# Optimization experiments

Measured on AMD Instinct MI355X. Metric: run time of the kernel, lower is better.

Reference implementation:

```python
import jax, jax.numpy as jnp
import numpy as np

B, L, D = 2, 2048, 1024
H, FD, HD = 16, 16, 64  # num_heads, feature_dim, head_dim
EPS = 1e-12


def setup_inputs() -> dict:
    key = jax.random.key(0)
    ks = jax.random.split(key, 5)
    s = 0.02
    return {
        "hidden_states": jax.random.normal(ks[0], (B, L, D), jnp.float32),
        "Wq": jax.random.normal(ks[1], (H * FD, D), jnp.float32) * s,
        "Wk": jax.random.normal(ks[2], (H * FD, D), jnp.float32) * s,
        "Wv": jax.random.normal(ks[3], (H * HD, D), jnp.float32) * s,
        "Wo": jax.random.normal(ks[4], (D, H * HD), jnp.float32) * s,
    }


def reference(hidden_states, Wq, Wk, Wv, Wo):
    b, l, _ = hidden_states.shape
    # projections (nn.Linear: y = x @ W.T), split heads -> (b, h, l, d)
    q = (hidden_states @ Wq.T).reshape(b, l, H, FD).transpose(0, 2, 1, 3)
    k = (hidden_states @ Wk.T).reshape(b, l, H, FD).transpose(0, 2, 1, 3)
    v = (hidden_states @ Wv.T).reshape(b, l, H, HD).transpose(0, 2, 1, 3)
    # feature_map is identity
    # quadratic causal linear attention
    A = jnp.einsum('bhnd,bhmd->bhnm', q, k)  # (b,h,l,l)
    causal = jnp.tril(jnp.ones((l, l), dtype=bool))
    A = jnp.where(causal, A, jnp.zeros((), A.dtype))
    y = jnp.einsum('bhnm,bhme->bhne', A, v)  # (b,h,l,hd)
    # causal cumsum normalization
    z = 1.0 / (jnp.einsum('bhld,bhld->bhl', q, jnp.cumsum(k, axis=2)) + EPS)
    y = y * z[..., None]
    y = y.transpose(0, 2, 1, 3).reshape(b, l, H * HD)  # b l (h d)
    return y @ Wo.T
```

## Files before the change

### kernel.cpp

```cpp
#include <hip/hip_runtime.h>


#define L_    2048
#define NROW  4096
#define CHUNK 128
#define NCH   16
#define NBH   32
#define K3    3072

typedef __attribute__((ext_vector_type(8))) short short8v;
typedef __attribute__((ext_vector_type(4))) float floatx4;

__device__ __forceinline__ ushort bf_rne(float x) {
    unsigned u = __float_as_uint(x);
    return (ushort)((u + 0x7fffu + ((u >> 16) & 1u)) >> 16);
}
__device__ __forceinline__ float bf_to_f(ushort h) {
    return __uint_as_float(((unsigned)h) << 16);
}
__device__ __forceinline__ void gload16(const ushort* g, ushort* l) {
    __builtin_amdgcn_global_load_lds(
        (const __attribute__((address_space(1))) unsigned int*)g,
        (__attribute__((address_space(3))) unsigned int*)l, 16, 0, 0);
}

__global__ __launch_bounds__(256) void split3(const float* __restrict__ in,
                                              ushort* __restrict__ out3, int nrow,
                                              int lo_off, int hi2_off) {
    int idx = blockIdx.x * 256 + threadIdx.x;
    int row = idx >> 7, g = idx & 127;
    if (row >= nrow) return;
    const float* p = in + (size_t)row * 1024 + g * 8;
    float4 x0 = *(const float4*)p, x1 = *(const float4*)(p + 4);
    float xs[8] = {x0.x, x0.y, x0.z, x0.w, x1.x, x1.y, x1.z, x1.w};
    ushort hs[8], ls[8];
#pragma unroll
    for (int j = 0; j < 8; ++j) {
        ushort h = bf_rne(xs[j]);
        hs[j] = h;
        ls[j] = bf_rne(xs[j] - bf_to_f(h));
    }
    ushort* o = out3 + (size_t)row * 3072 + g * 8;
    ushort4 h0 = make_ushort4(hs[0], hs[1], hs[2], hs[3]);
    ushort4 h1 = make_ushort4(hs[4], hs[5], hs[6], hs[7]);
    *(ushort4*)(o)               = h0;
    *(ushort4*)(o + 4)           = h1;
    *(ushort4*)(o + hi2_off)     = h0;
    *(ushort4*)(o + hi2_off + 4) = h1;
    *(ushort4*)(o + lo_off)      = make_ushort4(ls[0], ls[1], ls[2], ls[3]);
    *(ushort4*)(o + lo_off + 4)  = make_ushort4(ls[4], ls[5], ls[6], ls[7]);
}

__global__ __launch_bounds__(256) void gemm_bf16x3(const ushort* __restrict__ A3,
                                                   const ushort* __restrict__ B3,
                                                   float* __restrict__ Cm, int Nn) {
    __shared__ ushort As[2][8192];
    __shared__ ushort Bs[2][8192];
    const int tid = threadIdx.x;
    const int lane = tid & 63;
    const int wy = tid >> 7;
    const int wx = (tid >> 6) & 1;
    const int m0 = blockIdx.y * 128;
    const int n0 = blockIdx.x * 128;

    const int arow = tid >> 3;
    const int aslot = (tid & 7) ^ (arow & 7);
    const ushort* pA[4];
    const ushort* pB[4];
#pragma unroll
    for (int i = 0; i < 4; ++i) {
        pA[i] = A3 + (size_t)(m0 + i * 32 + arow) * K3 + aslot * 8;
        pB[i] = B3 + (size_t)(n0 + i * 32 + arow) * K3 + aslot * 8;
    }

#define STAGE(buf, kk)                                              \
    do {                                                            \
        _Pragma("unroll") for (int i = 0; i < 4; ++i)               \
            gload16(pA[i] + (kk), &As[buf][i * 2048 + tid * 8]);    \
        _Pragma("unroll") for (int i = 0; i < 4; ++i)               \
            gload16(pB[i] + (kk), &Bs[buf][i * 2048 + tid * 8]);    \
    } while (0)

    const int abase = (wy * 64 + (lane & 15)) * 64;
    const int bbase = (wx * 64 + (lane & 15)) * 64;

    floatx4 acc[4][4] = {};
    STAGE(0, 0);
    for (int t = 0; t < 48; ++t) {
        const int cur = t & 1;
        __syncthreads();
        if (t < 47) STAGE(1 - cur, (t + 1) * 64);
#pragma unroll
        for (int ksub = 0; ksub < 2; ++ksub) {
            const int so = ((((lane >> 4) | (ksub << 2)) ^ (lane & 7)) << 3);
            short8v a[4], b[4];
#pragma unroll
            for (int mf = 0; mf < 4; ++mf)
                a[mf] = *(const short8v*)&As[cur][abase + mf * 1024 + so];
#pragma unroll
            for (int nf = 0; nf < 4; ++nf)
                b[nf] = *(const short8v*)&Bs[cur][bbase + nf * 1024 + so];
#pragma unroll
            for (int mf = 0; mf < 4; ++mf)
#pragma unroll
                for (int nf = 0; nf < 4; ++nf)
                    acc[mf][nf] = __builtin_amdgcn_mfma_f32_16x16x32_bf16(
                        a[mf], b[nf], acc[mf][nf], 0, 0, 0);
        }
    }
#undef STAGE

#pragma unroll
    for (int mf = 0; mf < 4; ++mf) {
        int row = m0 + wy * 64 + mf * 16 + ((lane >> 4) << 2);
#pragma unroll
        for (int nf = 0; nf < 4; ++nf) {
            int col = n0 + wx * 64 + nf * 16 + (lane & 15);
#pragma unroll
            for (int r = 0; r < 4; ++r)
                Cm[(size_t)(row + r) * Nn + col] = acc[mf][nf][r];
        }
    }
}

#define TM 64
#define TN 64
#define TK 32
#define LDP 68

__global__ __launch_bounds__(256) void gemm_qk_f64(const float* __restrict__ X,
                                                   const float* __restrict__ Wq,
                                                   const float* __restrict__ Wk,
                                                   double* __restrict__ q64,
                                                   double* __restrict__ k64) {
    __shared__ float As[TK][LDP];
    __shared__ float Bs[TK][LDP];
    const int tid = threadIdx.x;
    const int m0 = blockIdx.y * TM;
    const int n0g = blockIdx.x * TN;
    const bool isq = n0g < 256;
    const float* Wm = isq ? Wq : Wk;
    double* Cm = isq ? q64 : k64;
    const int n0 = isq ? n0g : n0g - 256;

    const int lr = tid >> 2;
    const int lc = (tid & 3) << 2;
    const int ty = tid >> 4;
    const int tx = tid & 15;

    double acc[4][4] = {};
    const float* Ap = X + (size_t)(m0 + lr) * 1024 + lc;
    const float* Bp = Wm + (size_t)(n0 + lr) * 1024 + lc;

    for (int k0 = 0; k0 < 1024; k0 += TK) {
        float4 a0 = *(const float4*)(Ap + k0);
        float4 a1 = *(const float4*)(Ap + k0 + 16);
        float4 b0 = *(const float4*)(Bp + k0);
        float4 b1 = *(const float4*)(Bp + k0 + 16);
        __syncthreads();
        As[lc + 0][lr] = a0.x; As[lc + 1][lr] = a0.y;
        As[lc + 2][lr] = a0.z; As[lc + 3][lr] = a0.w;
        As[lc + 16][lr] = a1.x; As[lc + 17][lr] = a1.y;
        As[lc + 18][lr] = a1.z; As[lc + 19][lr] = a1.w;
        Bs[lc + 0][lr] = b0.x; Bs[lc + 1][lr] = b0.y;
        Bs[lc + 2][lr] = b0.z; Bs[lc + 3][lr] = b0.w;
        Bs[lc + 16][lr] = b1.x; Bs[lc + 17][lr] = b1.y;
        Bs[lc + 18][lr] = b1.z; Bs[lc + 19][lr] = b1.w;
        __syncthreads();
#pragma unroll
        for (int kk = 0; kk < TK; ++kk) {
            float4 av = *(const float4*)&As[kk][ty << 2];
            float4 bv = *(const float4*)&Bs[kk][tx << 2];
            double a[4] = {(double)av.x, (double)av.y, (double)av.z, (double)av.w};
            double b[4] = {(double)bv.x, (double)bv.y, (double)bv.z, (double)bv.w};
#pragma unroll
            for (int i = 0; i < 4; ++i)
#pragma unroll
                for (int j = 0; j < 4; ++j)
                    acc[i][j] += a[i] * b[j];
        }
    }
#pragma unroll
    for (int i = 0; i < 4; ++i) {
        size_t o = (size_t)(m0 + (ty << 2) + i) * 256 + n0 + (tx << 2);
        double2 r0 = {acc[i][0], acc[i][1]};
        double2 r1 = {acc[i][2], acc[i][3]};
        *(double2*)&Cm[o] = r0;
        *(double2*)&Cm[o + 2] = r1;
    }
}

__global__ __launch_bounds__(256) void chunk_kv(const double* __restrict__ kg,
                                                const float* __restrict__ vg,
                                                float* __restrict__ KV,
                                                double* __restrict__ Ksum) {
    __shared__ double ksd[CHUNK][16];
    __shared__ float vs[CHUNK][64];
    const int c = blockIdx.x, bh = blockIdx.y;
    const int b = bh >> 4, h = bh & 15;
    const int n0 = b * L_ + c * CHUNK;
    const int tid = threadIdx.x;

    {
        int r = tid >> 1, o = (tid & 1) * 8;
        const double* kp = &kg[(size_t)(n0 + r) * 256 + h * 16 + o];
#pragma unroll
        for (int j = 0; j < 4; ++j)
            *(double2*)&ksd[r][o + j * 2] = *(const double2*)(kp + j * 2);
    }
    {
        int r = tid >> 1, half = (tid & 1) * 32;
        const float* vp = &vg[(size_t)(n0 + r) * 1024 + h * 64 + half];
#pragma unroll
        for (int j = 0; j < 8; ++j)
            *(float4*)&vs[r][half + j * 4] = *(const float4*)(vp + j * 4);
    }
    __syncthreads();

    const int f = tid >> 4;
    const int e4 = tid & 15;
    float a0 = 0.f, a1 = 0.f, a2 = 0.f, a3 = 0.f;
    double ksacc = 0.0;
    for (int l = 0; l < CHUNK; ++l) {
        double kd = ksd[l][f];
        float kv = (float)kd;
        float4 vv = *(const float4*)&vs[l][e4 << 2];
        a0 += kv * vv.x; a1 += kv * vv.y; a2 += kv * vv.z; a3 += kv * vv.w;
        ksacc += kd;
    }
    size_t o = ((size_t)bh * NCH + c) * 1024 + f * 64 + (e4 << 2);
    float4 r = {a0, a1, a2, a3};
    *(float4*)&KV[o] = r;
    if (e4 == 0) Ksum[((size_t)bh * NCH + c) * 16 + f] = ksacc;
}

__global__ __launch_bounds__(256) void prefix_kv(const float* __restrict__ KV,
                                                 const double* __restrict__ Ksum,
                                                 float* __restrict__ KVpre,
                                                 double* __restrict__ Kpre) {
    const int bh = blockIdx.x;
    const int t = threadIdx.x;
    float r0 = 0.f, r1 = 0.f, r2 = 0.f, r3 = 0.f;
    size_t base = (size_t)bh * NCH * 1024 + t * 4;
    for (int c = 0; c < NCH; ++c) {
        float4 w = {r0, r1, r2, r3};
        *(float4*)&KVpre[base + (size_t)c * 1024] = w;
        float4 cur = *(const float4*)&KV[base + (size_t)c * 1024];
        r0 += cur.x; r1 += cur.y; r2 += cur.z; r3 += cur.w;
    }
    if (t < 16) {
        double s = 0.0;
        size_t kb = (size_t)bh * NCH * 16 + t;
        for (int c = 0; c < NCH; ++c) {
            Kpre[kb + (size_t)c * 16] = s;
            s += Ksum[kb + (size_t)c * 16];
        }
    }
}

__global__ __launch_bounds__(256) void attn_out(const double* __restrict__ qg,
                                                const double* __restrict__ kg,
                                                const float* __restrict__ vg,
                                                const float* __restrict__ kvpre,
                                                const double* __restrict__ kpreg,
                                                ushort* __restrict__ y3) {
    __shared__ double qs[CHUNK][16];
    __shared__ double ks[CHUNK][16];
    __shared__ float vs[CHUNK][64];
    __shared__ float s0[16][64];
    __shared__ double kp[16];
    const int c = blockIdx.x, bh = blockIdx.y;
    const int b = bh >> 4, h = bh & 15;
    const int n0 = b * L_ + c * CHUNK;
    const int tid = threadIdx.x;

    {
        int r = tid >> 1, o = (tid & 1) * 8;
        const double* qp = &qg[(size_t)(n0 + r) * 256 + h * 16 + o];
        const double* kptr = &kg[(size_t)(n0 + r) * 256 + h * 16 + o];
#pragma unroll
        for (int j = 0; j < 4; ++j) {
            *(double2*)&qs[r][o + j * 2] = *(const double2*)(qp + j * 2);
            *(double2*)&ks[r][o + j * 2] = *(const double2*)(kptr + j * 2);
        }
    }
    {
        int r = tid >> 1, half = (tid & 1) * 32;
        const float* vp = &vg[(size_t)(n0 + r) * 1024 + h * 64 + half];
#pragma unroll
        for (int j = 0; j < 8; ++j)
            *(float4*)&vs[r][half + j * 4] = *(const float4*)(vp + j * 4);
    }
    {
        float4 w = *(const float4*)&kvpre[((size_t)bh * NCH + c) * 1024 + tid * 4];
        *(float4*)&s0[0][tid * 4] = w;
        if (tid < 16) kp[tid] = kpreg[((size_t)bh * NCH + c) * 16 + tid];
    }
    __syncthreads();

    const int i = tid >> 1;
    const int half = (tid & 1) * 32;

    double qr[16];
#pragma unroll
    for (int f = 0; f < 16; ++f) qr[f] = qs[i][f];

    double denom = 0.0;
#pragma unroll
    for (int f = 0; f < 16; ++f) denom += qr[f] * kp[f];

    float acc[32] = {};
#pragma unroll
    for (int f = 0; f < 16; ++f) {
        float qf = (float)qr[f];
#pragma unroll
        for (int e = 0; e < 32; e += 4) {
            float4 sv = *(const float4*)&s0[f][half + e];
            acc[e + 0] += qf * sv.x; acc[e + 1] += qf * sv.y;
            acc[e + 2] += qf * sv.z; acc[e + 3] += qf * sv.w;
        }
    }
    for (int j = 0; j <= i; ++j) {
        double s64 = 0.0;
#pragma unroll
        for (int f = 0; f < 16; ++f) s64 += qr[f] * ks[j][f];
        denom += s64;
        float s = (float)s64;
        const float4* vj = (const float4*)&vs[j][half];
#pragma unroll
        for (int e4 = 0; e4 < 8; ++e4) {
            float4 vv = vj[e4];
            acc[e4 * 4 + 0] += s * vv.x; acc[e4 * 4 + 1] += s * vv.y;
            acc[e4 * 4 + 2] += s * vv.z; acc[e4 * 4 + 3] += s * vv.w;
        }
    }

    const float z = (float)(1.0 / (denom + 1e-12));
    ushort* yp = &y3[(size_t)(n0 + i) * K3 + h * 64 + half];
#pragma unroll
    for (int e4 = 0; e4 < 8; ++e4) {
        ushort hs[4], ls[4];
#pragma unroll
        for (int j = 0; j < 4; ++j) {
            float val = acc[e4 * 4 + j] * z;
            ushort hh = bf_rne(val);
            hs[j] = hh;
            ls[j] = bf_rne(val - bf_to_f(hh));
        }
        ushort4 hv = make_ushort4(hs[0], hs[1], hs[2], hs[3]);
        *(ushort4*)(yp + e4 * 4)        = hv;
        *(ushort4*)(yp + 1024 + e4 * 4) = make_ushort4(ls[0], ls[1], ls[2], ls[3]);
        *(ushort4*)(yp + 2048 + e4 * 4) = hv;
    }
}

extern "C" void kernel_launch(void* const* d_in, const int* in_sizes, int n_in,
                              void* d_out, int out_size, void* d_ws, size_t ws_size,
                              hipStream_t stream) {
    const float* X  = (const float*)d_in[0];
    const float* Wq = (const float*)d_in[1];
    const float* Wk = (const float*)d_in[2];
    const float* Wv = (const float*)d_in[3];
    const float* Wo = (const float*)d_in[4];
    float* out = (float*)d_out;

    double* q64   = (double*)d_ws;
    double* k64   = q64 + 1048576;
    float*  v     = (float*)(k64 + 1048576);
    float*  KV    = v + 4194304;
    float*  KVpre = KV + 524288;
    double* Ksum  = (double*)(KVpre + 524288);
    double* Kpre  = Ksum + 8192;
    ushort* X3    = (ushort*)(Kpre + 8192);
    ushort* Wv3   = X3 + (size_t)4096 * K3;
    ushort* Wo3   = Wv3 + (size_t)1024 * K3;

    dim3 blk(256);
    split3<<<2048, blk, 0, stream>>>(X, X3, 4096, 1024, 2048);
    split3<<<512, blk, 0, stream>>>(Wv, Wv3, 1024, 2048, 1024);
    split3<<<512, blk, 0, stream>>>(Wo, Wo3, 1024, 2048, 1024);
    gemm_qk_f64<<<dim3(8, 64), blk, 0, stream>>>(X, Wq, Wk, q64, k64);
    gemm_bf16x3<<<dim3(8, 32), blk, 0, stream>>>(X3, Wv3, v, 1024);
    chunk_kv<<<dim3(NCH, NBH), blk, 0, stream>>>(k64, v, KV, Ksum);
    prefix_kv<<<dim3(NBH), blk, 0, stream>>>(KV, Ksum, KVpre, Kpre);
    attn_out<<<dim3(NCH, NBH), blk, 0, stream>>>(q64, k64, v, KVpre, Kpre, X3);
    gemm_bf16x3<<<dim3(8, 32), blk, 0, stream>>>(X3, Wo3, out, 1024);
}
```

Baseline: 335.0 us.

## Merge fp64 QK projection and bf16x3 V projection into one heterogeneous launch

The separate fp64 Q/K GEMM and the bf16x3 MFMA V GEMM are combined into a single 768-block kernel. Blocks are interleaved in triples, two running the fp64 QK tile and one running the V tile, so the FP64-ALU-bound and MFMA-bound work share the GPU at the same time and one launch disappears. The cost is that every block now reserves 64 KB of shared memory, which limits occupancy for the QK blocks that only need a small part of it. Register pressure is also set by whichever of the two paths is larger.

```diff
diff --git a/kernel.cpp b/kernel.cpp
--- a/kernel.cpp
+++ b/kernel.cpp
@@ -7,6 +7,11 @@
 #define NCH   16
 #define NBH   32
 #define K3    3072
+
+#define TM 64
+#define TN 64
+#define TK 32
+#define LDP 68
 
 typedef __attribute__((ext_vector_type(8))) short short8v;
 typedef __attribute__((ext_vector_type(4))) float floatx4;
@@ -123,70 +128,144 @@
     }
 }
 
-#define TM 64
-#define TN 64
-#define TK 32
-#define LDP 68
-
-__global__ __launch_bounds__(256) void gemm_qk_f64(const float* __restrict__ X,
-                                                   const float* __restrict__ Wq,
-                                                   const float* __restrict__ Wk,
-                                                   double* __restrict__ q64,
-                                                   double* __restrict__ k64) {
-    __shared__ float As[TK][LDP];
-    __shared__ float Bs[TK][LDP];
+__global__ __launch_bounds__(256) void fused_qk_v(const float* __restrict__ X,
+                                                  const float* __restrict__ Wq,
+                                                  const float* __restrict__ Wk,
+                                                  double* __restrict__ q64,
+                                                  double* __restrict__ k64,
+                                                  const ushort* __restrict__ A3,
+                                                  const ushort* __restrict__ B3,
+                                                  float* __restrict__ Vout) {
+    __shared__ __align__(16) char smem[65536];
     const int tid = threadIdx.x;
-    const int m0 = blockIdx.y * TM;
-    const int n0g = blockIdx.x * TN;
-    const bool isq = n0g < 256;
-    const float* Wm = isq ? Wq : Wk;
-    double* Cm = isq ? q64 : k64;
-    const int n0 = isq ? n0g : n0g - 256;
-
-    const int lr = tid >> 2;
-    const int lc = (tid & 3) << 2;
-    const int ty = tid >> 4;
-    const int tx = tid & 15;
-
-    double acc[4][4] = {};
-    const float* Ap = X + (size_t)(m0 + lr) * 1024 + lc;
-    const float* Bp = Wm + (size_t)(n0 + lr) * 1024 + lc;
-
-    for (int k0 = 0; k0 < 1024; k0 += TK) {
-        float4 a0 = *(const float4*)(Ap + k0);
-        float4 a1 = *(const float4*)(Ap + k0 + 16);
-        float4 b0 = *(const float4*)(Bp + k0);
-        float4 b1 = *(const float4*)(Bp + k0 + 16);
-        __syncthreads();
-        As[lc + 0][lr] = a0.x; As[lc + 1][lr] = a0.y;
-        As[lc + 2][lr] = a0.z; As[lc + 3][lr] = a0.w;
-        As[lc + 16][lr] = a1.x; As[lc + 17][lr] = a1.y;
-        As[lc + 18][lr] = a1.z; As[lc + 19][lr] = a1.w;
-        Bs[lc + 0][lr] = b0.x; Bs[lc + 1][lr] = b0.y;
-        Bs[lc + 2][lr] = b0.z; Bs[lc + 3][lr] = b0.w;
-        Bs[lc + 16][lr] = b1.x; Bs[lc + 17][lr] = b1.y;
-        Bs[lc + 18][lr] = b1.z; Bs[lc + 19][lr] = b1.w;
-        __syncthreads();
-#pragma unroll
-        for (int kk = 0; kk < TK; ++kk) {
-            float4 av = *(const float4*)&As[kk][ty << 2];
-            float4 bv = *(const float4*)&Bs[kk][tx << 2];
-            double a[4] = {(double)av.x, (double)av.y, (double)av.z, (double)av.w};
-            double b[4] = {(double)bv.x, (double)bv.y, (double)bv.z, (double)bv.w};
-#pragma unroll
-            for (int i = 0; i < 4; ++i)
-#pragma unroll
-                for (int j = 0; j < 4; ++j)
-                    acc[i][j] += a[i] * b[j];
-        }
-    }
-#pragma unroll
-    for (int i = 0; i < 4; ++i) {
-        size_t o = (size_t)(m0 + (ty << 2) + i) * 256 + n0 + (tx << 2);
-        double2 r0 = {acc[i][0], acc[i][1]};
-        double2 r1 = {acc[i][2], acc[i][3]};
-        *(double2*)&Cm[o] = r0;
-        *(double2*)&Cm[o + 2] = r1;
+    const int bid = blockIdx.x;
+    const int trip = bid / 3;
+    const int r3 = bid - trip * 3;
+
+    if (r3 < 2) {
+        const int qkid = trip * 2 + r3;
+        float (*As)[LDP] = (float (*)[LDP])smem;
+        float (*Bs)[LDP] = (float (*)[LDP])(smem + sizeof(float) * TK * LDP);
+        const int m0 = (qkid >> 3) * TM;
+        const int n0g = (qkid & 7) * TN;
+        const bool isq = n0g < 256;
+        const float* Wm = isq ? Wq : Wk;
+        double* Cm = isq ? q64 : k64;
+        const int n0 = isq ? n0g : n0g - 256;
+
+        const int lr = tid >> 2;
+        const int lc = (tid & 3) << 2;
+        const int ty = tid >> 4;
+        const int tx = tid & 15;
+
+        double acc[4][4] = {};
+        const float* Ap = X + (size_t)(m0 + lr) * 1024 + lc;
+        const float* Bp = Wm + (size_t)(n0 + lr) * 1024 + lc;
+
+        for (int k0 = 0; k0 < 1024; k0 += TK) {
+            float4 a0 = *(const float4*)(Ap + k0);
+            float4 a1 = *(const float4*)(Ap + k0 + 16);
+            float4 b0 = *(const float4*)(Bp + k0);
+            float4 b1 = *(const float4*)(Bp + k0 + 16);
+            __syncthreads();
+            As[lc + 0][lr] = a0.x; As[lc + 1][lr] = a0.y;
+            As[lc + 2][lr] = a0.z; As[lc + 3][lr] = a0.w;
+            As[lc + 16][lr] = a1.x; As[lc + 17][lr] = a1.y;
+            As[lc + 18][lr] = a1.z; As[lc + 19][lr] = a1.w;
+            Bs[lc + 0][lr] = b0.x; Bs[lc + 1][lr] = b0.y;
+            Bs[lc + 2][lr] = b0.z; Bs[lc + 3][lr] = b0.w;
+            Bs[lc + 16][lr] = b1.x; Bs[lc + 17][lr] = b1.y;
+            Bs[lc + 18][lr] = b1.z; Bs[lc + 19][lr] = b1.w;
+            __syncthreads();
+#pragma unroll
+            for (int kk = 0; kk < TK; ++kk) {
+                float4 av = *(const float4*)&As[kk][ty << 2];
+                float4 bv = *(const float4*)&Bs[kk][tx << 2];
+                double a[4] = {(double)av.x, (double)av.y, (double)av.z, (double)av.w};
+                double b[4] = {(double)bv.x, (double)bv.y, (double)bv.z, (double)bv.w};
+#pragma unroll
+                for (int i = 0; i < 4; ++i)
+#pragma unroll
+                    for (int j = 0; j < 4; ++j)
+                        acc[i][j] += a[i] * b[j];
+            }
+        }
+#pragma unroll
+        for (int i = 0; i < 4; ++i) {
+            size_t o = (size_t)(m0 + (ty << 2) + i) * 256 + n0 + (tx << 2);
+            double2 r0 = {acc[i][0], acc[i][1]};
+            double2 r1 = {acc[i][2], acc[i][3]};
+            *(double2*)&Cm[o] = r0;
+            *(double2*)&Cm[o + 2] = r1;
+        }
+    } else {
+        const int vid = trip;
+        ushort (*As2)[8192] = (ushort (*)[8192])smem;
+        ushort (*Bs2)[8192] = (ushort (*)[8192])(smem + 32768);
+        const int lane = tid & 63;
+        const int wy = tid >> 7;
+        const int wx = (tid >> 6) & 1;
+        const int m0 = (vid >> 3) * 128;
+        const int n0 = (vid & 7) * 128;
+
+        const int arow = tid >> 3;
+        const int aslot = (tid & 7) ^ (arow & 7);
+        const ushort* pA[4];
+        const ushort* pB[4];
+#pragma unroll
+        for (int i = 0; i < 4; ++i) {
+            pA[i] = A3 + (size_t)(m0 + i * 32 + arow) * K3 + aslot * 8;
+            pB[i] = B3 + (size_t)(n0 + i * 32 + arow) * K3 + aslot * 8;
+        }
+
+#define STAGE2(buf, kk)                                              \
+    do {                                                             \
+        _Pragma("unroll") for (int i = 0; i < 4; ++i)                \
+            gload16(pA[i] + (kk), &As2[buf][i * 2048 + tid * 8]);    \
+        _Pragma("unroll") for (int i = 0; i < 4; ++i)                \
+            gload16(pB[i] + (kk), &Bs2[buf][i * 2048 + tid * 8]);    \
+    } while (0)
+
+        const int abase = (wy * 64 + (lane & 15)) * 64;
+        const int bbase = (wx * 64 + (lane & 15)) * 64;
+
+        floatx4 acc[4][4] = {};
+        STAGE2(0, 0);
+        for (int t = 0; t < 48; ++t) {
+            const int cur = t & 1;
+            __syncthreads();
+            if (t < 47) STAGE2(1 - cur, (t + 1) * 64);
+#pragma unroll
+            for (int ksub = 0; ksub < 2; ++ksub) {
+                const int so = ((((lane >> 4) | (ksub << 2)) ^ (lane & 7)) << 3);
+                short8v a[4], b[4];
+#pragma unroll
+                for (int mf = 0; mf < 4; ++mf)
+                    a[mf] = *(const short8v*)&As2[cur][abase + mf * 1024 + so];
+#pragma unroll
+                for (int nf = 0; nf < 4; ++nf)
+                    b[nf] = *(const short8v*)&Bs2[cur][bbase + nf * 1024 + so];
+#pragma unroll
+                for (int mf = 0; mf < 4; ++mf)
+#pragma unroll
+                    for (int nf = 0; nf < 4; ++nf)
+                        acc[mf][nf] = __builtin_amdgcn_mfma_f32_16x16x32_bf16(
+                            a[mf], b[nf], acc[mf][nf], 0, 0, 0);
+            }
+        }
+#undef STAGE2
+
+#pragma unroll
+        for (int mf = 0; mf < 4; ++mf) {
+            int row = m0 + wy * 64 + mf * 16 + ((lane >> 4) << 2);
+#pragma unroll
+            for (int nf = 0; nf < 4; ++nf) {
+                int col = n0 + wx * 64 + nf * 16 + (lane & 15);
+#pragma unroll
+                for (int r = 0; r < 4; ++r)
+                    Vout[(size_t)(row + r) * 1024 + col] = acc[mf][nf][r];
+            }
+        }
     }
 }
 
@@ -379,8 +458,7 @@
     split3<<<2048, blk, 0, stream>>>(X, X3, 4096, 1024, 2048);
     split3<<<512, blk, 0, stream>>>(Wv, Wv3, 1024, 2048, 1024);
     split3<<<512, blk, 0, stream>>>(Wo, Wo3, 1024, 2048, 1024);
-    gemm_qk_f64<<<dim3(8, 64), blk, 0, stream>>>(X, Wq, Wk, q64, k64);
-    gemm_bf16x3<<<dim3(8, 32), blk, 0, stream>>>(X3, Wv3, v, 1024);
+    fused_qk_v<<<768, blk, 0, stream>>>(X, Wq, Wk, q64, k64, X3, Wv3, v);
     chunk_kv<<<dim3(NCH, NBH), blk, 0, stream>>>(k64, v, KV, Ksum);
     prefix_kv<<<dim3(NBH), blk, 0, stream>>>(KV, Ksum, KVpre, Kpre);
     attn_out<<<dim3(NCH, NBH), blk, 0, stream>>>(q64, k64, v, KVpre, Kpre, X3);
```

Result: slower. 365.8 us (+9.2%).
